# Performance work log

Hardware: AMD Instinct MI355X
Metric: run time of the kernel (lower is better)

## Reference

```python
import jax, jax.numpy as jnp
import numpy as np

B, N, EP = 128, 1024, 8192          # graphs, nodes/graph, edges/graph
E = B * EP
K1, K2 = 820, 656                   # ceil(0.8*1024), ceil(0.8*820)
H = 120                             # GRU hidden
L = 101                             # target sequence length

def _w(k, shape, s=0.05):
    return jax.random.normal(k, shape, jnp.float32) * s

def setup_inputs():
    ks = jax.random.split(jax.random.key(0), 16)
    rng = np.random.default_rng(0)
    off = np.arange(B)[:, None] * N
    src = (rng.integers(0, N, size=(B, EP)) + off).reshape(-1).astype(np.int32)
    dst = (rng.integers(0, N, size=(B, EP)) + off).reshape(-1).astype(np.int32)
    return dict(
        x=jax.random.normal(ks[0], (B * N, 4), jnp.float32),
        target=jax.random.normal(ks[1], (B, 30, L), jnp.float32),
        edge_src=jnp.asarray(src), edge_dst=jnp.asarray(dst),
        W1_rel=_w(ks[2], (4, 128)), W1_root=_w(ks[3], (4, 128)), b1=jnp.zeros((128,)),
        p1=_w(ks[4], (128,), 1.0),
        W2_rel=_w(ks[5], (128, 128)), W2_root=_w(ks[6], (128, 128)), b2=jnp.zeros((128,)),
        p2=_w(ks[7], (128,), 1.0),
        Wc=_w(ks[8], (128, 30, 3)), bc=jnp.zeros((128,)),
        Wih_f=_w(ks[9], (3 * H, 128)), Whh_f=_w(ks[10], (3 * H, H)),
        bih_f=jnp.zeros((3 * H,)), bhh_f=jnp.zeros((3 * H,)),
        Wih_b=_w(ks[11], (3 * H, 128)), Whh_b=_w(ks[12], (3 * H, H)),
        bih_b=jnp.zeros((3 * H,)), bhh_b=jnp.zeros((3 * H,)),
        Wd1=_w(ks[13], (4816, 102)), bd1=jnp.zeros((102,)),
        Wd3=_w(ks[14], (102, 2)), bd3=jnp.zeros((2,)),
    )

def _gconv(x, src, dst, valid, n, Wrel, Wroot, b):
    # PyG GraphConv: lin_rel(sum_{j->i} x_j) + lin_root(x_i)
    m = x[src] * valid[:, None]                       # [E,F] gather + edge mask
    agg = jax.ops.segment_sum(m, dst, num_segments=n)  # scatter-add
    return agg @ Wrel + x @ Wroot + b

def _topk_pool(x, src, dst, valid, n_per, k, p):
    # PyG TopKPooling: score = tanh(x.p/||p||); keep top-k per graph; x *= score
    score = jnp.tanh(x @ p / jnp.linalg.norm(p))      # [B*n_per]
    _, idx = jax.lax.top_k(score.reshape(B, n_per), k)
    perm = (idx + jnp.arange(B)[:, None] * n_per).reshape(-1)  # [B*k] global ids
    new_x = x[perm] * score[perm][:, None]
    mapping = jnp.full((B * n_per,), -1, jnp.int32).at[perm].set(
        jnp.arange(B * k, dtype=jnp.int32))
    ns, nd = mapping[src], mapping[dst]
    nv = valid & (ns >= 0) & (nd >= 0)                # edges with both ends kept
    return new_x, jnp.maximum(ns, 0), jnp.maximum(nd, 0), nv

def _readout(x, k):
    xr = x.reshape(B, k, 128)
    return jnp.concatenate([xr.max(1), xr.mean(1)], axis=1)  # gmp || gap -> [B,256]

def _gru_dir(xs, Wih, Whh, bih, bhh):                 # xs: [T,B,128]
    def step(h, xt):
        gi = xt @ Wih.T + bih
        gh = h @ Whh.T + bhh
        ir, iz, inn = jnp.split(gi, 3, -1)
        hr, hz, hn = jnp.split(gh, 3, -1)
        r = jax.nn.sigmoid(ir + hr)
        z = jax.nn.sigmoid(iz + hz)
        ng = jnp.tanh(inn + r * hn)
        hnew = (1.0 - z) * ng + z * h
        return hnew, hnew
    h0 = jnp.zeros((xs.shape[1], H), xs.dtype)
    return jax.lax.scan(step, h0, xs)[1]              # [T,B,H]

def _forward(params, edge_src, edge_dst):
    (x, target, W1_rel, W1_root, b1, p1, W2_rel, W2_root, b2, p2, Wc, bc,
     Wih_f, Whh_f, bih_f, bhh_f, Wih_b, Whh_b, bih_b, bhh_b,
     Wd1, bd1, Wd3, bd3) = params
    valid0 = jnp.ones((E,), bool)
    h = jax.nn.relu(_gconv(x, edge_src, edge_dst, valid0, B * N, W1_rel, W1_root, b1))
    h, s1, d1, v1 = _topk_pool(h, edge_src, edge_dst, valid0, N, K1, p1)
    x1 = _readout(h, K1)
    h = jax.nn.relu(_gconv(h, s1, d1, v1, B * K1, W2_rel, W2_root, b2))
    h, s2, d2, v2 = _topk_pool(h, s1, d1, v1, K1, K2, p2)
    x2 = _readout(h, K2)
    xg = x1 + x2                                      # [B,256]
    # target branch (dropout = identity in eval mode)
    xt = jax.lax.conv_general_dilated(target, Wc, (1,), 'VALID',
                                      dimension_numbers=('NCH', 'OIH', 'NCH'))
    xt = jax.nn.relu(xt + bc[None, :, None])          # [B,128,99]
    xt = xt[:, :, :95].reshape(B, 128, 19, 5).mean(-1)  # avg_pool1d(k=5,s=5)
    xs = xt.transpose(2, 0, 1)                        # [T=19,B,128]
    yf = _gru_dir(xs, Wih_f, Whh_f, bih_f, bhh_f)
    yb = _gru_dir(xs[::-1], Wih_b, Whh_b, bih_b, bhh_b)[::-1]
    y = jnp.concatenate([yf, yb], -1).transpose(1, 0, 2).reshape(B, -1)  # [B,4560]
    xc = jnp.concatenate([xg, y], 1)                  # [B,4816]
    xc = jax.nn.relu(xc @ Wd1 + bd1)
    return jax.nn.log_softmax(xc @ Wd3 + bd3, axis=-1)

def reference(x, target, edge_src, edge_dst, W1_rel, W1_root, b1, p1,
              W2_rel, W2_root, b2, p2, Wc, bc, Wih_f, Whh_f, bih_f, bhh_f,
              Wih_b, Whh_b, bih_b, bhh_b, Wd1, bd1, Wd3, bd3):
    params = (x, target, W1_rel, W1_root, b1, p1, W2_rel, W2_root, b2, p2,
              Wc, bc, Wih_f, Whh_f, bih_f, bhh_f, Wih_b, Whh_b, bih_b, bhh_b,
              Wd1, bd1, Wd3, bd3)
    return _forward(params, edge_src, edge_dst)
```

## Files before the change

kernel.cpp:

```cpp
#include <hip/hip_runtime.h>
#include <math.h>

#define BB   128
#define NN   1024
#define BN   (BB*NN)
#define EDG  (BB*8192)
#define K1C  820
#define K2C  656
#define TSEQ 19
#define HID  120
#define D1K  4816
#define D1CH 76
#define NCH2 11

typedef unsigned short u16;
typedef __attribute__((ext_vector_type(8))) short bf16x8;
typedef __attribute__((ext_vector_type(4))) float f32x4;

__device__ __forceinline__ u16 f2b(float x) {
  unsigned int u = __float_as_uint(x);
  u += 0x7FFFu + ((u >> 16) & 1u);
  return (u16)(u >> 16);
}
__device__ __forceinline__ float b2f(u16 v) {
  return __uint_as_float(((unsigned int)v) << 16);
}

__device__ __forceinline__ float blockReduceSum128(float v, float* tmp2) {
#pragma unroll
  for (int o = 32; o > 0; o >>= 1) v += __shfl_down(v, o);
  int lane = threadIdx.x & 63, w = threadIdx.x >> 6;
  if (lane == 0) tmp2[w] = v;
  __syncthreads();
  float r = tmp2[0] + tmp2[1];
  __syncthreads();
  return r;
}

__global__ void k_pnorm(const float* __restrict__ p1, const float* __restrict__ p2,
                        float* __restrict__ invp) {
  __shared__ float tmp2[2];
  float a = p1[threadIdx.x], b = p2[threadIdx.x];
  float s1 = blockReduceSum128(a * a, tmp2);
  float s2 = blockReduceSum128(b * b, tmp2);
  if (threadIdx.x == 0) { invp[0] = 1.f / sqrtf(s1); invp[1] = 1.f / sqrtf(s2); }
}

__global__ void k_wb(const float* __restrict__ W2rel, const float* __restrict__ W2root,
                     u16* __restrict__ Wfrag) {
  int idx = blockIdx.x * 256 + threadIdx.x;
  int lane = idx & 63, ct = (idx >> 6) & 7, ks = idx >> 9;
  int c = ct * 16 + (lane & 15);
  int kbase = ks * 32 + (lane >> 4) * 8;
#pragma unroll
  for (int j = 0; j < 8; ++j) {
    int k = kbase + j;
    float w = (k < 128) ? W2rel[(size_t)k * 128 + c] : W2root[(size_t)(k - 128) * 128 + c];
    Wfrag[(size_t)idx * 8 + j] = f2b(w);
  }
}

__global__ __launch_bounds__(1024) void k_l1(const int* __restrict__ src,
                                             const int* __restrict__ dst,
                                             const float* __restrict__ x,
                                             float* __restrict__ agg1) {
  __shared__ int hcur[1024];
  __shared__ int sscan[1024];
  __shared__ int ccnt[1024];
  __shared__ int el[8192];
  __shared__ float4 xls4[1024];
  int b = blockIdx.x, tid = threadIdx.x;
  int base = b * 8192, nb = b * 1024;
  hcur[tid] = 0;
  __syncthreads();
#pragma unroll
  for (int it = 0; it < 8; ++it)
    atomicAdd(&hcur[dst[base + it * 1024 + tid] - nb], 1);
  __syncthreads();
  int v = hcur[tid];
  ccnt[tid] = v;
  sscan[tid] = v;
  __syncthreads();
  for (int o = 1; o < 1024; o <<= 1) {
    int t = (tid >= o) ? sscan[tid - o] : 0;
    __syncthreads();
    sscan[tid] += t;
    __syncthreads();
  }
  hcur[tid] = sscan[tid] - v;
  __syncthreads();
#pragma unroll
  for (int it = 0; it < 8; ++it) {
    int e = base + it * 1024 + tid;
    int d = dst[e] - nb;
    int pos = atomicAdd(&hcur[d], 1);
    el[pos] = src[e] - nb;
  }
  xls4[tid] = ((const float4*)x)[nb + tid];
  __syncthreads();
  const float* xls = (const float*)xls4;
  int rg = tid >> 2, lane = tid & 3;
#pragma unroll
  for (int it = 0; it < 4; ++it) {
    int r = rg + it * 256;
    int n = ccnt[r], s0 = sscan[r] - n;
    float a0 = 0.f, a1 = 0.f;
    int j = 0;
    for (; j + 1 < n; j += 2) {
      a0 += xls[el[s0 + j] * 4 + lane];
      a1 += xls[el[s0 + j + 1] * 4 + lane];
    }
    if (j < n) a0 += xls[el[s0 + j] * 4 + lane];
    agg1[(size_t)(nb + r) * 4 + lane] = a0 + a1;
  }
}

__global__ void k_h1(const float* __restrict__ x, const float* __restrict__ agg1,
                     const float* __restrict__ W1rel, const float* __restrict__ W1root,
                     const float* __restrict__ b1, const float* __restrict__ p1,
                     const float* __restrict__ invp,
                     float* __restrict__ h1, float* __restrict__ score1) {
  int tid = blockIdx.x * 256 + threadIdx.x;
  int r = tid >> 5, lane = tid & 31, f4 = lane * 4;
  float4 a = ((const float4*)agg1)[r];
  float4 xv = ((const float4*)x)[r];
  float o[4], dot = 0.f;
#pragma unroll
  for (int j = 0; j < 4; ++j) {
    int f = f4 + j;
    float acc = b1[f]
      + a.x * W1rel[f] + a.y * W1rel[128 + f] + a.z * W1rel[256 + f] + a.w * W1rel[384 + f]
      + xv.x * W1root[f] + xv.y * W1root[128 + f] + xv.z * W1root[256 + f] + xv.w * W1root[384 + f];
    o[j] = fmaxf(acc, 0.f);
    dot += o[j] * p1[f];
  }
  *(float4*)&h1[(size_t)r * 128 + f4] = make_float4(o[0], o[1], o[2], o[3]);
#pragma unroll
  for (int off = 16; off > 0; off >>= 1) dot += __shfl_down(dot, off, 32);
  if (lane == 0) score1[r] = tanhf(dot * invp[0]);
}

__global__ __launch_bounds__(1024) void k_sort(const float* __restrict__ score, int n_per, int K,
                       int* __restrict__ perm, int* __restrict__ mapping) {
  __shared__ float s[1024];
  __shared__ int   id[1024];
  int b = blockIdx.x;
  const float* sc = score + (size_t)b * n_per;
  for (int i = threadIdx.x; i < 1024; i += blockDim.x) {
    if (i < n_per) { s[i] = sc[i]; id[i] = i; }
    else           { s[i] = -INFINITY; id[i] = 0x7fffffff; }
  }
  __syncthreads();
  for (int k = 2; k <= 1024; k <<= 1) {
    for (int j = k >> 1; j > 0; j >>= 1) {
      for (int i = threadIdx.x; i < 1024; i += blockDim.x) {
        int l = i ^ j;
        if (l > i) {
          float si = s[i], sl = s[l];
          int ii = id[i], il = id[l];
          bool iBeforeL = (si > sl) || (si == sl && ii < il);
          bool up = ((i & k) == 0);
          if (up ? (!iBeforeL) : iBeforeL) {
            s[i] = sl; s[l] = si; id[i] = il; id[l] = ii;
          }
        }
      }
      __syncthreads();
    }
  }
  for (int r = threadIdx.x; r < K; r += blockDim.x)
    perm[(size_t)b * K + r] = b * n_per + id[r];
  if (mapping) {
    for (int i = threadIdx.x; i < n_per; i += blockDim.x)
      mapping[(size_t)b * n_per + i] = -1;
    __syncthreads();
    for (int r = threadIdx.x; r < K; r += blockDim.x)
      mapping[(size_t)b * n_per + id[r]] = b * K + r;
  }
}

#define RCH 64
__global__ void k_gatherread(const u16* __restrict__ h2b, const float* __restrict__ score,
                             const int* __restrict__ perm,
                             float* __restrict__ pmax, float* __restrict__ psum,
                             int K, int nch) {
  int b = blockIdx.x / nch, c = blockIdx.x % nch, f = threadIdx.x;
  int r0 = c * RCH, r1 = min(r0 + RCH, K);
  float mx = -INFINITY, sm = 0.f;
  for (int r = r0; r < r1; ++r) {
    int g = perm[(size_t)b * K + r];
    float v = b2f(h2b[(size_t)g * 128 + f]) * score[g];
    mx = fmaxf(mx, v); sm += v;
  }
  pmax[((size_t)b * nch + c) * 128 + f] = mx;
  psum[((size_t)b * nch + c) * 128 + f] = sm;
}

__global__ __launch_bounds__(1024) void k_csr2(const int* __restrict__ src,
                                               const int* __restrict__ dst,
                                               const int* __restrict__ map,
                                               int* __restrict__ starts2,
                                               int* __restrict__ cnt2,
                                               int* __restrict__ elist2) {
  __shared__ int mloc[8192];
  __shared__ int msl[8192];
  __shared__ int h[1024];
  __shared__ int s[1024];
  int g = blockIdx.x, tid = threadIdx.x;
  int base = g * 8192, nb2 = g * K1C;
  h[tid] = 0;
  __syncthreads();
#pragma unroll
  for (int it = 0; it < 8; ++it) {
    int e = base + it * 1024 + tid;
    int ms = map[src[e]], md = map[dst[e]];
    bool valid = (ms >= 0) && (md >= 0);
    int idx = it * 1024 + tid;
    int ml = valid ? (md - nb2) : -1;
    mloc[idx] = ml;
    msl[idx] = ms - nb2;
    if (valid) atomicAdd(&h[ml], 1);
  }
  __syncthreads();
  int v = (tid < K1C) ? h[tid] : 0;
  if (tid < K1C) cnt2[nb2 + tid] = v;
  s[tid] = v;
  __syncthreads();
  for (int o = 1; o < 1024; o <<= 1) {
    int t = (tid >= o) ? s[tid - o] : 0;
    __syncthreads();
    s[tid] += t;
    __syncthreads();
  }
  int st = s[tid] - v;
  if (tid < K1C) starts2[nb2 + tid] = base + st;
  h[tid] = st;
  __syncthreads();
#pragma unroll
  for (int it = 0; it < 8; ++it) {
    int idx = it * 1024 + tid;
    int ml = mloc[idx];
    if (ml >= 0) {
      int pos = atomicAdd(&h[ml], 1);
      elist2[base + pos] = msl[idx];
    }
  }
}

__global__ __launch_bounds__(1024) void k_agg2r(const int* __restrict__ starts2,
                                                const int* __restrict__ cnt2,
                                                const int* __restrict__ elist2,
                                                const int* __restrict__ perm1,
                                                const float* __restrict__ score1,
                                                const float* __restrict__ h1,
                                                u16* __restrict__ Abf,
                                                float* __restrict__ xmax1,
                                                float* __restrict__ xsum1) {
  __shared__ float xls[K1C * 32];
  __shared__ int   el[8192];
  __shared__ int   sts[K1C];
  __shared__ int   ctn[K1C];
  __shared__ int   pid[K1C];
  __shared__ float scs[K1C];
  __shared__ float redm[16][36];
  __shared__ float reds[16][36];
  int g = blockIdx.x >> 2, q = blockIdx.x & 3;
  int tid = threadIdx.x;
  int nb2 = g * K1C, base = g * 8192;
  for (int i = tid; i < K1C; i += 1024) {
    int p = perm1[nb2 + i];
    pid[i] = p;
    scs[i] = score1[p];
    sts[i] = starts2[nb2 + i] - base;
    ctn[i] = cnt2[nb2 + i];
  }
  {
    const int4* e4 = (const int4*)(elist2 + base);
    for (int i = tid; i < 2048; i += 1024) ((int4*)el)[i] = e4[i];
  }
  __syncthreads();
  for (int i = tid; i < K1C * 8; i += 1024) {
    int row = i >> 3, f4 = (i & 7) * 4;
    float4 v = *(const float4*)&h1[(size_t)pid[row] * 128 + q * 32 + f4];
    float s = scs[row];
    v.x *= s; v.y *= s; v.z *= s; v.w *= s;
    *(float4*)&xls[row * 32 + f4] = v;
    ushort4 bv;
    bv.x = f2b(v.x); bv.y = f2b(v.y); bv.z = f2b(v.z); bv.w = f2b(v.w);
    *(ushort4*)&Abf[(size_t)(nb2 + row) * 256 + 128 + q * 32 + f4] = bv;
  }
  __syncthreads();
  int rg = tid >> 3, f4l = (tid & 7) * 4;
  float4 mx = make_float4(-INFINITY, -INFINITY, -INFINITY, -INFINITY);
  float4 sm = make_float4(0.f, 0.f, 0.f, 0.f);
  for (int r = rg; r < K1C; r += 128) {
    int s0 = sts[r], n = ctn[r];
    float4 a = make_float4(0.f, 0.f, 0.f, 0.f);
    float4 c = make_float4(0.f, 0.f, 0.f, 0.f);
    int j = 0;
    for (; j + 1 < n; j += 2) {
      float4 v0 = *(const float4*)&xls[el[s0 + j] * 32 + f4l];
      float4 v1 = *(const float4*)&xls[el[s0 + j + 1] * 32 + f4l];
      a.x += v0.x; a.y += v0.y; a.z += v0.z; a.w += v0.w;
      c.x += v1.x; c.y += v1.y; c.z += v1.z; c.w += v1.w;
    }
    if (j < n) {
      float4 v = *(const float4*)&xls[el[s0 + j] * 32 + f4l];
      a.x += v.x; a.y += v.y; a.z += v.z; a.w += v.w;
    }
    ushort4 ov;
    ov.x = f2b(a.x + c.x); ov.y = f2b(a.y + c.y);
    ov.z = f2b(a.z + c.z); ov.w = f2b(a.w + c.w);
    *(ushort4*)&Abf[(size_t)(nb2 + r) * 256 + q * 32 + f4l] = ov;
    float4 w = *(const float4*)&xls[r * 32 + f4l];
    mx.x = fmaxf(mx.x, w.x); mx.y = fmaxf(mx.y, w.y);
    mx.z = fmaxf(mx.z, w.z); mx.w = fmaxf(mx.w, w.w);
    sm.x += w.x; sm.y += w.y; sm.z += w.z; sm.w += w.w;
  }
#pragma unroll
  for (int m = 8; m <= 32; m <<= 1) {
    mx.x = fmaxf(mx.x, __shfl_xor(mx.x, m)); mx.y = fmaxf(mx.y, __shfl_xor(mx.y, m));
    mx.z = fmaxf(mx.z, __shfl_xor(mx.z, m)); mx.w = fmaxf(mx.w, __shfl_xor(mx.w, m));
    sm.x += __shfl_xor(sm.x, m); sm.y += __shfl_xor(sm.y, m);
    sm.z += __shfl_xor(sm.z, m); sm.w += __shfl_xor(sm.w, m);
  }
  int wv = tid >> 6;
  if ((tid & 63) < 8) {
    *(float4*)&redm[wv][f4l] = mx;
    *(float4*)&reds[wv][f4l] = sm;
  }
  __syncthreads();
  if (tid < 32) {
    float m = redm[0][tid], s2 = reds[0][tid];
#pragma unroll
    for (int w2 = 1; w2 < 16; ++w2) {
      m = fmaxf(m, redm[w2][tid]);
      s2 += reds[w2][tid];
    }
    xmax1[g * 128 + q * 32 + tid] = m;
    xsum1[g * 128 + q * 32 + tid] = s2;
  }
}

__global__ __launch_bounds__(256, 4) void k_h2m(
    const u16* __restrict__ Abf, const u16* __restrict__ Wfrag,
    const float* __restrict__ b2, const float* __restrict__ p2,
    const float* __restrict__ invp,
    u16* __restrict__ h2b, float* __restrict__ score2) {
  __shared__ u16 Als[64][40];
  int tid = threadIdx.x;
  int r0 = blockIdx.x * 64;
  int wv = tid >> 6, lane = tid & 63;
  int lr = lane & 15, kg = lane >> 4;
  f32x4 acc[8];
  f32x4 z = {0.f, 0.f, 0.f, 0.f};
#pragma unroll
  for (int ct = 0; ct < 8; ++ct) acc[ct] = z;
  for (int ks = 0; ks < 8; ++ks) {
    {
      int row = tid >> 2, kq = (tid & 3) * 8;
      *(f32x4*)&Als[row][kq] =
          *(const f32x4*)&Abf[(size_t)(r0 + row) * 256 + ks * 32 + kq];
    }
    __syncthreads();
    bf16x8 a = *(const bf16x8*)&Als[wv * 16 + lr][kg * 8];
    const u16* wf = Wfrag + (size_t)ks * 4096;
#pragma unroll
    for (int ct = 0; ct < 8; ++ct) {
      bf16x8 b = *(const bf16x8*)&wf[(ct * 64 + lane) * 8];
      acc[ct] = __builtin_amdgcn_mfma_f32_16x16x32_bf16(a, b, acc[ct], 0, 0, 0);
    }
    __syncthreads();
  }
  float inv = invp[1];
  float dots[4] = {0.f, 0.f, 0.f, 0.f};
#pragma unroll
  for (int ct = 0; ct < 8; ++ct) {
    int c = ct * 16 + lr;
    float bb = b2[c], pp = p2[c];
#pragma unroll
    for (int i = 0; i < 4; ++i) {
      float o = fmaxf(acc[ct][i] + bb, 0.f);
      h2b[(size_t)(r0 + wv * 16 + kg * 4 + i) * 128 + c] = f2b(o);
      dots[i] += o * pp;
    }
  }
#pragma unroll
  for (int i = 0; i < 4; ++i) {
    float d = dots[i];
#pragma unroll
    for (int m = 8; m >= 1; m >>= 1) d += __shfl_xor(d, m);
    if (lr == 0) score2[r0 + wv * 16 + kg * 4 + i] = tanhf(d * inv);
  }
}

__global__ void k_conv(const float* __restrict__ target, const float* __restrict__ Wc,
                       const float* __restrict__ bc, float* __restrict__ xs) {
  int gb = blockIdx.x;
  int b = gb / TSEQ, tt = gb % TSEQ;
  int o = threadIdx.x;
  __shared__ float tg[30][8];
  for (int i = threadIdx.x; i < 210; i += 128) {
    int ch = i / 7, u = i % 7;
    tg[ch][u] = target[((size_t)b * 30 + ch) * 101 + tt * 5 + u];
  }
  __syncthreads();
  const float* w = Wc + (size_t)o * 90;
  float acc5[5] = {0, 0, 0, 0, 0};
  for (int ch = 0; ch < 30; ++ch) {
    float w0 = w[ch * 3], w1 = w[ch * 3 + 1], w2 = w[ch * 3 + 2];
#pragma unroll
    for (int u = 0; u < 5; ++u)
      acc5[u] += tg[ch][u] * w0 + tg[ch][u + 1] * w1 + tg[ch][u + 2] * w2;
  }
  float bo = bc[o], s = 0.f;
#pragma unroll
  for (int u = 0; u < 5; ++u) s += fmaxf(acc5[u] + bo, 0.f);
  xs[((size_t)tt * BB + b) * 128 + o] = s * 0.2f;
}

#define GIB 16
__global__ __launch_bounds__(384) void k_gi(const float* __restrict__ xs,
                     const float* __restrict__ Wihf, const float* __restrict__ bihf,
                     const float* __restrict__ Wihb, const float* __restrict__ bihb,
                     float* __restrict__ gi) {
  int bg = blockIdx.x & 7;
  int t = (blockIdx.x >> 3) % TSEQ;
  int dir = blockIdx.x / (8 * TSEQ);
  int b0 = bg * GIB;
  __shared__ float xst[GIB][128];
  int tid = threadIdx.x;
  for (int i = tid; i < GIB * 128; i += 384) {
    int bb = i >> 7, k = i & 127;
    xst[bb][k] = xs[((size_t)t * BB + b0 + bb) * 128 + k];
  }
  __syncthreads();
  int j = tid;
  if (j < 360) {
    const float* W = (dir ? Wihb : Wihf) + (size_t)j * 128;
    float bias = (dir ? bihb : bihf)[j];
    float acc[GIB];
#pragma unroll
    for (int bb = 0; bb < GIB; ++bb) acc[bb] = bias;
#pragma unroll 4
    for (int k = 0; k < 128; ++k) {
      float w = W[k];
#pragma unroll
      for (int bb = 0; bb < GIB; ++bb) acc[bb] += xst[bb][k] * w;
    }
    size_t base = ((size_t)dir * TSEQ + t) * BB + b0;
#pragma unroll
    for (int bb = 0; bb < GIB; ++bb) gi[(base + bb) * 360 + j] = acc[bb];
  }
}

__global__ __launch_bounds__(384) void k_gru(const float* __restrict__ gi,
                      const float* __restrict__ Whhf, const float* __restrict__ bhhf,
                      const float* __restrict__ Whhb, const float* __restrict__ bhhb,
                      float* __restrict__ xc) {
  int b = blockIdx.x & 127, dir = blockIdx.x >> 7;
  const float* Whh = dir ? Whhb : Whhf;
  const float* bhh = dir ? bhhb : bhhf;
  __shared__ float h_sh[HID];
  __shared__ float g_sh[360];
  int j = threadIdx.x;
  float wrow[HID];
  float bias = 0.f;
  if (j < 360) {
    const float4* W4 = (const float4*)(Whh + (size_t)j * HID);
#pragma unroll
    for (int k4 = 0; k4 < HID / 4; ++k4) {
      float4 w = W4[k4];
      wrow[k4 * 4 + 0] = w.x; wrow[k4 * 4 + 1] = w.y;
      wrow[k4 * 4 + 2] = w.z; wrow[k4 * 4 + 3] = w.w;
    }
    bias = bhh[j];
  }
  if (j < HID) h_sh[j] = 0.f;
  __syncthreads();
  for (int st = 0; st < TSEQ; ++st) {
    int tt = dir ? (TSEQ - 1 - st) : st;
    if (j < 360) {
      float a0 = bias;
      const float4* h4 = (const float4*)h_sh;
#pragma unroll
      for (int k4 = 0; k4 < HID / 4; ++k4) {
        float4 v0 = h4[k4];
        a0 += wrow[k4*4+0]*v0.x + wrow[k4*4+1]*v0.y + wrow[k4*4+2]*v0.z + wrow[k4*4+3]*v0.w;
      }
      g_sh[j] = a0;
    }
    __syncthreads();
    if (j < HID) {
      const float* g = gi + (((size_t)dir * TSEQ + tt) * BB + b) * 360;
      float r  = 1.f / (1.f + expf(-(g[j]       + g_sh[j])));
      float z  = 1.f / (1.f + expf(-(g[120 + j] + g_sh[120 + j])));
      float ng = tanhf(g[240 + j] + r * g_sh[240 + j]);
      float hn = (1.f - z) * ng + z * h_sh[j];
      h_sh[j] = hn;
      xc[(size_t)b * 4816 + 256 + (size_t)tt * 240 + dir * 120 + j] = hn;
    }
    __syncthreads();
  }
}

__global__ void k_xg(const float* __restrict__ xmax1, const float* __restrict__ xsum1,
                     const float* __restrict__ pmax2, const float* __restrict__ psum2,
                     float* __restrict__ xc) {
  int b = blockIdx.x, f = threadIdx.x;
  float mx2 = -INFINITY, sm2 = 0.f;
  for (int c = 0; c < NCH2; ++c) {
    mx2 = fmaxf(mx2, pmax2[((size_t)b * NCH2 + c) * 128 + f]);
    sm2 += psum2[((size_t)b * NCH2 + c) * 128 + f];
  }
  xc[(size_t)b * 4816 + f] = xmax1[b * 128 + f] + mx2;
  xc[(size_t)b * 4816 + 128 + f] = xsum1[b * 128 + f] / (float)K1C + sm2 / (float)K2C;
}

__global__ __launch_bounds__(128) void k_d1(const float* __restrict__ xc,
                                            const float* __restrict__ Wd1,
                                            float* __restrict__ part) {
  int c = blockIdx.x % D1CH;
  int rg = blockIdx.x / D1CH;
  int k0 = c * 64, kn = min(64, D1K - k0);
  __shared__ float wls[64 * 102];
  __shared__ float xcs[4][64];
  int tid = threadIdx.x;
  for (int i = tid; i < 4 * 64; i += 128) {
    int r = i >> 6, k = i & 63;
    xcs[r][k] = (k < kn) ? xc[(size_t)(rg * 4 + r) * D1K + k0 + k] : 0.f;
  }
  {
    const float2* s2 = (const float2*)(Wd1 + (size_t)k0 * 102);
    float2* d2 = (float2*)wls;
    int n2 = (kn * 102) >> 1;
    for (int i = tid; i < n2; i += 128) d2[i] = s2[i];
  }
  __syncthreads();
  int j = tid;
  if (j < 102) {
    float a0 = 0.f, a1 = 0.f, a2 = 0.f, a3 = 0.f;
#pragma unroll 4
    for (int k = 0; k < kn; ++k) {
      float w = wls[k * 102 + j];
      a0 += xcs[0][k] * w; a1 += xcs[1][k] * w;
      a2 += xcs[2][k] * w; a3 += xcs[3][k] * w;
    }
    part[((size_t)(rg * 4 + 0) * D1CH + c) * 102 + j] = a0;
    part[((size_t)(rg * 4 + 1) * D1CH + c) * 102 + j] = a1;
    part[((size_t)(rg * 4 + 2) * D1CH + c) * 102 + j] = a2;
    part[((size_t)(rg * 4 + 3) * D1CH + c) * 102 + j] = a3;
  }
}

__global__ void k_final2(const float* __restrict__ part, const float* __restrict__ bd1,
                         const float* __restrict__ Wd3, const float* __restrict__ bd3,
                         float* __restrict__ out) {
  __shared__ float tmp2[2];
  int b = blockIdx.x, j = threadIdx.x;
  float v = 0.f;
  if (j < 102) {
    const float* pb = part + (size_t)b * D1CH * 102 + j;
    float s0 = 0.f, s1 = 0.f, s2 = 0.f, s3 = 0.f;
    for (int c = 0; c < D1CH; c += 4) {
      s0 += pb[(c + 0) * 102];
      s1 += pb[(c + 1) * 102];
      s2 += pb[(c + 2) * 102];
      s3 += pb[(c + 3) * 102];
    }
    v = fmaxf((s0 + s1) + (s2 + s3) + bd1[j], 0.f);
  }
  float c0 = (j < 102) ? v * Wd3[j * 2] : 0.f;
  float c1 = (j < 102) ? v * Wd3[j * 2 + 1] : 0.f;
  float z0 = blockReduceSum128(c0, tmp2) + bd3[0];
  float z1 = blockReduceSum128(c1, tmp2) + bd3[1];
  if (j < 2) {
    float m = fmaxf(z0, z1);
    float lse = m + logf(expf(z0 - m) + expf(z1 - m));
    out[b * 2 + j] = (j == 0 ? z0 : z1) - lse;
  }
}

extern "C" void kernel_launch(void* const* d_in, const int* in_sizes, int n_in,
                              void* d_out, int out_size, void* d_ws, size_t ws_size,
                              hipStream_t stream) {
  const float* x      = (const float*)d_in[0];
  const float* target = (const float*)d_in[1];
  const int*   esrc   = (const int*)d_in[2];
  const int*   edst   = (const int*)d_in[3];
  const float* W1rel  = (const float*)d_in[4];
  const float* W1root = (const float*)d_in[5];
  const float* b1     = (const float*)d_in[6];
  const float* p1     = (const float*)d_in[7];
  const float* W2rel  = (const float*)d_in[8];
  const float* W2root = (const float*)d_in[9];
  const float* b2     = (const float*)d_in[10];
  const float* p2     = (const float*)d_in[11];
  const float* Wc     = (const float*)d_in[12];
  const float* bc     = (const float*)d_in[13];
  const float* Wihf   = (const float*)d_in[14];
  const float* Whhf   = (const float*)d_in[15];
  const float* bihf   = (const float*)d_in[16];
  const float* bhhf   = (const float*)d_in[17];
  const float* Wihb   = (const float*)d_in[18];
  const float* Whhb   = (const float*)d_in[19];
  const float* bihb   = (const float*)d_in[20];
  const float* bhhb   = (const float*)d_in[21];
  const float* Wd1    = (const float*)d_in[22];
  const float* bd1    = (const float*)d_in[23];
  const float* Wd3    = (const float*)d_in[24];
  const float* bd3    = (const float*)d_in[25];
  float* out = (float*)d_out;

  char* wsb = (char*)d_ws;
  size_t off = 0;
  auto alloc = [&](size_t bytes) -> void* {
    void* p = wsb + off;
    off = (off + bytes + 255) & ~(size_t)255;
    return p;
  };
  float* h1      = (float*)alloc((size_t)BN * 128 * 4);
  u16*   Abf     = (u16*)  alloc((size_t)BB * K1C * 256 * 2);
  u16*   Wfrag   = (u16*)  alloc((size_t)4096 * 8 * 2);
  float* agg1    = (float*)alloc((size_t)BN * 4 * 4);
  float* score1  = (float*)alloc((size_t)BN * 4);
  int*   perm1   = (int*)  alloc((size_t)BB * K1C * 4);
  int*   map1    = (int*)  alloc((size_t)BN * 4);
  u16*   h2b     = (u16*)  alloc((size_t)BB * K1C * 128 * 2);
  float* score2  = (float*)alloc((size_t)BB * K1C * 4);
  int*   perm2   = (int*)  alloc((size_t)BB * K2C * 4);
  float* invp    = (float*)alloc(256);
  float* xs      = (float*)alloc((size_t)TSEQ * BB * 128 * 4);
  float* gi      = (float*)alloc((size_t)2 * TSEQ * BB * 360 * 4);
  float* xc      = (float*)alloc((size_t)BB * 4816 * 4);
  int*   starts2 = (int*)  alloc((size_t)BB * K1C * 4);
  int*   cnt2    = (int*)  alloc((size_t)BB * K1C * 4);
  int*   elist2  = (int*)  alloc((size_t)EDG * 4);
  float* xmax1   = (float*)alloc((size_t)BB * 128 * 4);
  float* xsum1   = (float*)alloc((size_t)BB * 128 * 4);
  float* pmax2   = (float*)alloc((size_t)BB * NCH2 * 128 * 4);
  float* psum2   = (float*)alloc((size_t)BB * NCH2 * 128 * 4);
  float* part    = (float*)alloc((size_t)BB * D1CH * 102 * 4);

  k_pnorm<<<1, 128, 0, stream>>>(p1, p2, invp);
  k_wb<<<16, 256, 0, stream>>>(W2rel, W2root, Wfrag);

  k_l1<<<BB, 1024, 0, stream>>>(esrc, edst, x, agg1);
  k_h1<<<BN * 32 / 256, 256, 0, stream>>>(x, agg1, W1rel, W1root, b1, p1, invp, h1, score1);
  k_sort<<<BB, 1024, 0, stream>>>(score1, NN, K1C, perm1, map1);

  k_csr2<<<BB, 1024, 0, stream>>>(esrc, edst, map1, starts2, cnt2, elist2);
  k_agg2r<<<BB * 4, 1024, 0, stream>>>(starts2, cnt2, elist2, perm1, score1, h1,
                                       Abf, xmax1, xsum1);
  k_h2m<<<(BB * K1C) / 64, 256, 0, stream>>>(Abf, Wfrag, b2, p2, invp, h2b, score2);
  k_sort<<<BB, 1024, 0, stream>>>(score2, K1C, K2C, perm2, nullptr);
  k_gatherread<<<BB * NCH2, 128, 0, stream>>>(h2b, score2, perm2, pmax2, psum2, K2C, NCH2);

  k_conv<<<BB * TSEQ, 128, 0, stream>>>(target, Wc, bc, xs);
  k_gi<<<2 * TSEQ * 8, 384, 0, stream>>>(xs, Wihf, bihf, Wihb, bihb, gi);
  k_gru<<<2 * 128, 384, 0, stream>>>(gi, Whhf, bhhf, Whhb, bhhb, xc);

  k_xg<<<BB, 128, 0, stream>>>(xmax1, xsum1, pmax2, psum2, xc);
  k_d1<<<(BB / 4) * D1CH, 128, 0, stream>>>(xc, Wd1, part);
  k_final2<<<BB, 128, 0, stream>>>(part, bd1, Wd3, bd3, out);
}
```

Baseline: 273.8 us.

## Store h1 and edge lists in 16-bit, double-buffer A tiles in h2 MFMA

Writes the first-layer hidden features h1 as bf16 instead of fp32 and narrows the second-layer edge list to 16-bit local indices. This halves the bytes written by k_h1 and k_csr2 and read by k_agg2r, and shrinks the shared-memory edge buffer. k_h2m now double-buffers its A tile in shared memory, prefetching the next K-slice from global while the MFMAs run, which removes one barrier per step. The cost is extra bf16 rounding of h1 before the sort-gather and score scaling, which may perturb accuracy slightly.

```diff
diff --git a/kernel.cpp b/kernel.cpp
--- a/kernel.cpp
+++ b/kernel.cpp
@@ -119,7 +119,7 @@
                      const float* __restrict__ W1rel, const float* __restrict__ W1root,
                      const float* __restrict__ b1, const float* __restrict__ p1,
                      const float* __restrict__ invp,
-                     float* __restrict__ h1, float* __restrict__ score1) {
+                     u16* __restrict__ h1b, float* __restrict__ score1) {
   int tid = blockIdx.x * 256 + threadIdx.x;
   int r = tid >> 5, lane = tid & 31, f4 = lane * 4;
   float4 a = ((const float4*)agg1)[r];
@@ -134,7 +134,9 @@
     o[j] = fmaxf(acc, 0.f);
     dot += o[j] * p1[f];
   }
-  *(float4*)&h1[(size_t)r * 128 + f4] = make_float4(o[0], o[1], o[2], o[3]);
+  ushort4 hv;
+  hv.x = f2b(o[0]); hv.y = f2b(o[1]); hv.z = f2b(o[2]); hv.w = f2b(o[3]);
+  *(ushort4*)&h1b[(size_t)r * 128 + f4] = hv;
 #pragma unroll
   for (int off = 16; off > 0; off >>= 1) dot += __shfl_down(dot, off, 32);
   if (lane == 0) score1[r] = tanhf(dot * invp[0]);
@@ -201,7 +203,7 @@
                                                const int* __restrict__ map,
                                                int* __restrict__ starts2,
                                                int* __restrict__ cnt2,
-                                               int* __restrict__ elist2) {
+                                               u16* __restrict__ elist2) {
   __shared__ int mloc[8192];
   __shared__ int msl[8192];
   __shared__ int h[1024];
@@ -242,22 +244,22 @@
     int ml = mloc[idx];
     if (ml >= 0) {
       int pos = atomicAdd(&h[ml], 1);
-      elist2[base + pos] = msl[idx];
+      elist2[base + pos] = (u16)msl[idx];
     }
   }
 }
 
 __global__ __launch_bounds__(1024) void k_agg2r(const int* __restrict__ starts2,
                                                 const int* __restrict__ cnt2,
-                                                const int* __restrict__ elist2,
+                                                const u16* __restrict__ elist2,
                                                 const int* __restrict__ perm1,
                                                 const float* __restrict__ score1,
-                                                const float* __restrict__ h1,
+                                                const u16* __restrict__ h1b,
                                                 u16* __restrict__ Abf,
                                                 float* __restrict__ xmax1,
                                                 float* __restrict__ xsum1) {
   __shared__ float xls[K1C * 32];
-  __shared__ int   el[8192];
+  __shared__ u16   el[8192];
   __shared__ int   sts[K1C];
   __shared__ int   ctn[K1C];
   __shared__ int   pid[K1C];
@@ -276,14 +278,16 @@
   }
   {
     const int4* e4 = (const int4*)(elist2 + base);
-    for (int i = tid; i < 2048; i += 1024) ((int4*)el)[i] = e4[i];
+    if (tid < 1024) ((int4*)el)[tid] = e4[tid];
   }
   __syncthreads();
   for (int i = tid; i < K1C * 8; i += 1024) {
     int row = i >> 3, f4 = (i & 7) * 4;
-    float4 v = *(const float4*)&h1[(size_t)pid[row] * 128 + q * 32 + f4];
+    ushort4 hv = *(const ushort4*)&h1b[(size_t)pid[row] * 128 + q * 32 + f4];
     float s = scs[row];
-    v.x *= s; v.y *= s; v.z *= s; v.w *= s;
+    float4 v;
+    v.x = b2f(hv.x) * s; v.y = b2f(hv.y) * s;
+    v.z = b2f(hv.z) * s; v.w = b2f(hv.w) * s;
     *(float4*)&xls[row * 32 + f4] = v;
     ushort4 bv;
     bv.x = f2b(v.x); bv.y = f2b(v.y); bv.z = f2b(v.z); bv.w = f2b(v.w);
@@ -347,30 +351,33 @@
     const float* __restrict__ b2, const float* __restrict__ p2,
     const float* __restrict__ invp,
     u16* __restrict__ h2b, float* __restrict__ score2) {
-  __shared__ u16 Als[64][40];
+  __shared__ u16 Als[2][64][40];
   int tid = threadIdx.x;
   int r0 = blockIdx.x * 64;
   int wv = tid >> 6, lane = tid & 63;
   int lr = lane & 15, kg = lane >> 4;
+  int row = tid >> 2, kq = (tid & 3) * 8;
   f32x4 acc[8];
   f32x4 z = {0.f, 0.f, 0.f, 0.f};
 #pragma unroll
   for (int ct = 0; ct < 8; ++ct) acc[ct] = z;
+  f32x4 st = *(const f32x4*)&Abf[(size_t)(r0 + row) * 256 + 0 * 32 + kq];
+  *(f32x4*)&Als[0][row][kq] = st;
+  __syncthreads();
+  int cur = 0;
   for (int ks = 0; ks < 8; ++ks) {
-    {
-      int row = tid >> 2, kq = (tid & 3) * 8;
-      *(f32x4*)&Als[row][kq] =
-          *(const f32x4*)&Abf[(size_t)(r0 + row) * 256 + ks * 32 + kq];
-    }
-    __syncthreads();
-    bf16x8 a = *(const bf16x8*)&Als[wv * 16 + lr][kg * 8];
+    if (ks < 7)
+      st = *(const f32x4*)&Abf[(size_t)(r0 + row) * 256 + (ks + 1) * 32 + kq];
+    bf16x8 a = *(const bf16x8*)&Als[cur][wv * 16 + lr][kg * 8];
     const u16* wf = Wfrag + (size_t)ks * 4096;
 #pragma unroll
     for (int ct = 0; ct < 8; ++ct) {
       bf16x8 b = *(const bf16x8*)&wf[(ct * 64 + lane) * 8];
       acc[ct] = __builtin_amdgcn_mfma_f32_16x16x32_bf16(a, b, acc[ct], 0, 0, 0);
     }
-    __syncthreads();
+    if (ks < 7) *(f32x4*)&Als[cur ^ 1][row][kq] = st;
+    __syncthreads();
+    cur ^= 1;
   }
   float inv = invp[1];
   float dots[4] = {0.f, 0.f, 0.f, 0.f};
@@ -619,7 +626,7 @@
     off = (off + bytes + 255) & ~(size_t)255;
     return p;
   };
-  float* h1      = (float*)alloc((size_t)BN * 128 * 4);
+  u16*   h1b     = (u16*)  alloc((size_t)BN * 128 * 2);
   u16*   Abf     = (u16*)  alloc((size_t)BB * K1C * 256 * 2);
   u16*   Wfrag   = (u16*)  alloc((size_t)4096 * 8 * 2);
   float* agg1    = (float*)alloc((size_t)BN * 4 * 4);
@@ -635,7 +642,7 @@
   float* xc      = (float*)alloc((size_t)BB * 4816 * 4);
   int*   starts2 = (int*)  alloc((size_t)BB * K1C * 4);
   int*   cnt2    = (int*)  alloc((size_t)BB * K1C * 4);
-  int*   elist2  = (int*)  alloc((size_t)EDG * 4);
+  u16*   elist2  = (u16*)  alloc((size_t)EDG * 2);
   float* xmax1   = (float*)alloc((size_t)BB * 128 * 4);
   float* xsum1   = (float*)alloc((size_t)BB * 128 * 4);
   float* pmax2   = (float*)alloc((size_t)BB * NCH2 * 128 * 4);
@@ -646,11 +653,11 @@
   k_wb<<<16, 256, 0, stream>>>(W2rel, W2root, Wfrag);
 
   k_l1<<<BB, 1024, 0, stream>>>(esrc, edst, x, agg1);
-  k_h1<<<BN * 32 / 256, 256, 0, stream>>>(x, agg1, W1rel, W1root, b1, p1, invp, h1, score1);
+  k_h1<<<BN * 32 / 256, 256, 0, stream>>>(x, agg1, W1rel, W1root, b1, p1, invp, h1b, score1);
   k_sort<<<BB, 1024, 0, stream>>>(score1, NN, K1C, perm1, map1);
 
   k_csr2<<<BB, 1024, 0, stream>>>(esrc, edst, map1, starts2, cnt2, elist2);
-  k_agg2r<<<BB * 4, 1024, 0, stream>>>(starts2, cnt2, elist2, perm1, score1, h1,
+  k_agg2r<<<BB * 4, 1024, 0, stream>>>(starts2, cnt2, elist2, perm1, score1, h1b,
                                        Abf, xmax1, xsum1);
   k_h2m<<<(BB * K1C) / 64, 256, 0, stream>>>(Abf, Wfrag, b2, p2, invp, h2b, score2);
   k_sort<<<BB, 1024, 0, stream>>>(score2, K1C, K2C, perm2, nullptr);
```

After: 294.4 us. 7.5% more time.
